# Kernel tuning notes

Hardware: AMD Instinct MI355X
Metric: run time of the kernel (lower is better)

Reference implementation:

```python
import jax, jax.numpy as jnp
import numpy as np

N, T, D, C = 32, 512, 1024, 120
EPS = 1e-12
SCALE = 2.0 * (D ** 0.5)


def setup_inputs() -> dict:
    key = jax.random.key(0)
    ks = jax.random.split(key, 16)
    inp = {
        'anc_perm_input': jax.random.normal(ks[0], (N, T, D), dtype=jnp.float32),
        'pos_perm_input': jax.random.normal(ks[1], (N, T, D), dtype=jnp.float32),
        'neg_perm_input': jax.random.normal(ks[2], (N, T, D), dtype=jnp.float32),
        'anc_src_key_padding_mask': jax.random.randint(ks[3], (N, T), 0, 2) == 1,
        'pos_src_key_padding_mask': jax.random.randint(ks[4], (N, T), 0, 2) == 1,
        'neg_src_key_padding_mask': jax.random.randint(ks[5], (N, T), 0, 2) == 1,
        # learned parameters (stored as (in, out); math-equivalent to torch x @ W.T)
        'W_attn': jax.random.normal(ks[6], (D, D), dtype=jnp.float32) * 0.02,
        'b_attn': jnp.zeros((D,), dtype=jnp.float32),
        'W1': jax.random.normal(ks[7], (D, D), dtype=jnp.float32) * 0.02,
        'b1': jnp.zeros((D,), dtype=jnp.float32),
        'W2': jax.random.normal(ks[8], (D, D), dtype=jnp.float32) * 0.02,
        'b2': jnp.zeros((D,), dtype=jnp.float32),
        'ln_g': jnp.ones((D,), dtype=jnp.float32),
        'ln_b': jnp.zeros((D,), dtype=jnp.float32),
        'W_last': jax.random.normal(ks[9], (D, C), dtype=jnp.float32) * 0.02,
        'b_last': jnp.zeros((C,), dtype=jnp.float32),
    }
    return inp


def _ntd_nd(x, mask, W_attn, b_attn, W1, b1, W2, b2, ln_g, ln_b, W_last, b_last):
    # x: (N,T,D); mask: (N,T) bool, True = padding
    w = x @ W_attn + b_attn                                   # (N,T,D)
    valid = ~mask                                             # (N,T)
    scores = jnp.einsum('btd,bsd->bts', w, w)                 # (N,T,T)
    scores = jnp.where(valid[:, :, None] & valid[:, None, :], scores, 0.0)
    s = jnp.sum(scores, axis=1) / SCALE                       # (N,T)
    s = jnp.where(mask, -jnp.inf, s)
    attn = jax.nn.softmax(s, axis=1)                          # (N,T)
    # proj_head: duplicate OrderedDict key => linear1 -> relu -> linear2 (no final act)
    proj = jax.nn.relu(x @ W1 + b1) @ W2 + b2                 # (N,T,D)
    pooled = jnp.einsum('bt,btd->bd', attn, proj)             # (N,D)
    mu = jnp.mean(pooled, axis=-1, keepdims=True)
    var = jnp.var(pooled, axis=-1, keepdims=True)
    normed = (pooled - mu) / jnp.sqrt(var + EPS) * ln_g + ln_b
    return jax.nn.relu(normed) @ W_last + b_last              # (N,C)


def reference(anc_perm_input, pos_perm_input, neg_perm_input,
              anc_src_key_padding_mask, pos_src_key_padding_mask, neg_src_key_padding_mask,
              W_attn, b_attn, W1, b1, W2, b2, ln_g, ln_b, W_last, b_last):
    params = (W_attn, b_attn, W1, b1, W2, b2, ln_g, ln_b, W_last, b_last)
    anc = _ntd_nd(anc_perm_input, anc_src_key_padding_mask, *params)
    pos = _ntd_nd(pos_perm_input, pos_src_key_padding_mask, *params)
    neg = _ntd_nd(neg_perm_input, neg_src_key_padding_mask, *params)
    return (anc, pos, neg)
```

## Files before the change

### kernel.cpp

```cpp
#include <hip/hip_runtime.h>
#include <hip/hip_bf16.h>
#include <math.h>

#define N_B 32
#define T_S 512
#define D_D 1024
#define C_C 120
#define ZB 96
#define SCALE 64.0f

typedef unsigned short u16;
typedef __attribute__((ext_vector_type(8))) short short8;
typedef __attribute__((ext_vector_type(8))) unsigned short ushort8;
typedef __attribute__((ext_vector_type(4))) float floatx4;

__device__ inline u16 f2bf(float f) {
    union { __hip_bfloat16 h; u16 u; } c; c.h = __float2bfloat16(f); return c.u;
}
__device__ inline float bf2f(u16 u) {
    union { unsigned i; float f; } c; c.i = ((unsigned)u) << 16; return c.f;
}

__device__ inline void gll16(const void* g, void* l) {
    __builtin_amdgcn_global_load_lds((const __attribute__((address_space(1))) void*)g,
                                     (__attribute__((address_space(3))) void*)l,
                                     16, 0, 0);
}

__device__ inline bool mask_is_i8(const int* mk) {
    bool i8 = false;
#pragma unroll
    for (int i = 0; i < 16; i++) {
        unsigned v = ((const unsigned*)mk)[i];
        if (v > 1u) i8 = true;
    }
    return i8;
}
__device__ inline int mask_val(const int* mk, int idx, bool i8) {
    return i8 ? (int)((const signed char*)mk)[idx] : mk[idx];
}

__global__ void k_scan(const int* m0, const int* m1, const int* m2,
                       int* __restrict__ chunk_base, int* __restrict__ cnts,
                       u16* __restrict__ xp, float4* __restrict__ zreg) {
    int zb = blockIdx.x;
    int tid = threadIdx.x;
    {
        float4 zz4 = {0.f, 0.f, 0.f, 0.f};
        for (int i = zb * 256 + tid; i < (2 * 1024 * 1024 / 16); i += ZB * 256)
            zreg[i] = zz4;
    }
    int z = zb >> 5, b = zb & 31;
    const int* mk = z == 0 ? m0 : (z == 1 ? m1 : m2);
    bool i8 = mask_is_i8(mk);
    __shared__ int wcnt[8];
    bool v0 = (mask_val(mk, b * T_S + tid, i8) == 0);
    bool v1 = (mask_val(mk, b * T_S + 256 + tid, i8) == 0);
    unsigned long long b0 = __ballot(v0);
    unsigned long long b1 = __ballot(v1);
    int wave = tid >> 6;
    if ((tid & 63) == 0) {
        wcnt[wave] = (int)__popcll(b0);
        wcnt[wave + 4] = (int)__popcll(b1);
    }
    __syncthreads();
    __shared__ int s_cnt;
    if (tid == 0) {
        int run = 0;
#pragma unroll
        for (int c = 0; c < 8; c++) {
            chunk_base[zb * 8 + c] = run;
            run += wcnt[c];
        }
        cnts[zb] = run;
        s_cnt = run;
    }
    __syncthreads();
    int cnt = s_cnt;
    int cend = (cnt + 255) & ~255;
    if (cend > T_S) cend = T_S;
    u16* base = xp + ((size_t)zb * T_S + cnt) * D_D;
    int n8 = (cend - cnt) * (D_D / 8);
    ushort8 zz = {0,0,0,0,0,0,0,0};
    for (int i = tid; i < n8; i += 256)
        *(ushort8*)(base + (size_t)i * 8) = zz;
}

__global__ void k_prep(const float* __restrict__ W_attn, const float* __restrict__ W1,
                       const float* x0, const float* x1, const float* x2,
                       const int* m0, const int* m1, const int* m2,
                       const int* __restrict__ chunk_base,
                       float* __restrict__ WT, u16* __restrict__ W1T,
                       float* __restrict__ xsum, u16* __restrict__ xp) {
    int bx = blockIdx.x;
    int tid = threadIdx.x;
    if (bx < 1024) {
        int tbx = bx & 31, tby = bx >> 5;
        __shared__ float tile[32][33];
        int tx = tid & 31, ty = tid >> 5;
#pragma unroll
        for (int j = 0; j < 32; j += 8)
            tile[ty + j][tx] = W_attn[(size_t)(tby*32 + ty + j)*D_D + tbx*32 + tx];
        __syncthreads();
#pragma unroll
        for (int j = 0; j < 32; j += 8)
            WT[(size_t)(tbx*32 + ty + j)*D_D + tby*32 + tx] = tile[tx][ty + j];
        __syncthreads();
#pragma unroll
        for (int j = 0; j < 32; j += 8)
            tile[ty + j][tx] = W1[(size_t)(tby*32 + ty + j)*D_D + tbx*32 + tx];
        __syncthreads();
#pragma unroll
        for (int j = 0; j < 32; j += 8)
            W1T[(size_t)(tbx*32 + ty + j)*D_D + tby*32 + tx] = f2bf(tile[tx][ty + j]);
        return;
    }
    int idx = bx - 1024;
    int chunk = idx & 7, zb = idx >> 3;
    int z = zb >> 5, b = zb & 31;
    const float* x = z == 0 ? x0 : (z == 1 ? x1 : x2);
    const int* mk = z == 0 ? m0 : (z == 1 ? m1 : m2);
    bool i8 = mask_is_i8(mk);
    int t0 = chunk * 64;
    __shared__ unsigned char s_list[64];
    __shared__ int s_cc;
    if (tid < 64) {
        bool v = (mask_val(mk, b * T_S + t0 + tid, i8) == 0);
        unsigned long long bal = __ballot(v);
        int pos = (int)__popcll(bal & ((1ull << tid) - 1ull));
        if (v) s_list[pos] = (unsigned char)tid;
        if (tid == 0) s_cc = (int)__popcll(bal);
    }
    __syncthreads();
    int cc = s_cc;
    int slot0 = chunk_base[zb * 8 + chunk];
    const float4* xr = (const float4*)(x + (size_t)(b * T_S) * D_D);
    u16* pack = xp + (size_t)zb * T_S * D_D;
    float4 acc = {0.f, 0.f, 0.f, 0.f};
#pragma unroll 2
    for (int j = 0; j < cc; j++) {
        int t = t0 + (int)s_list[j];
        float4 v = xr[(size_t)t * 256 + tid];
        union { __hip_bfloat162 h; ushort2 u; } c0, c1;
        c0.h = __float22bfloat162_rn({v.x, v.y});
        c1.h = __float22bfloat162_rn({v.z, v.w});
        ushort4 uu = {c0.u.x, c0.u.y, c1.u.x, c1.u.y};
        *(ushort4*)(pack + (size_t)(slot0 + j) * D_D + tid * 4) = uu;
        acc.x += v.x; acc.y += v.y; acc.z += v.z; acc.w += v.w;
    }
    float* xs = xsum + (size_t)zb * D_D + tid * 4;
    atomicAdd(xs + 0, acc.x); atomicAdd(xs + 1, acc.y);
    atomicAdd(xs + 2, acc.z); atomicAdd(xs + 3, acc.w);
}

__global__ void k_matvec(const float* __restrict__ W, const float* __restrict__ vin,
                         const float* __restrict__ bias, const int* __restrict__ bmul,
                         float scale, float* __restrict__ vout) {
    int z = blockIdx.z, bg = blockIdx.y;
    int och = blockIdx.x >> 3, kc = blockIdx.x & 7;
    int o = och * 256 + threadIdx.x;
    int brow = z * N_B + bg * 4;
    float acc[4] = {0.f, 0.f, 0.f, 0.f};
    if (kc == 0 && bias) {
        float bv = bias[o];
#pragma unroll
        for (int bb = 0; bb < 4; bb++)
            acc[bb] = bmul ? bv * (float)bmul[brow + bb] : bv;
    }
    const float* vi = vin + (size_t)brow * D_D + kc * 128;
    const float* Wp = W + (size_t)(kc * 128) * D_D + o;
#pragma unroll 4
    for (int i = 0; i < 128; i++) {
        float wv = Wp[(size_t)i * D_D];
#pragma unroll
        for (int bb = 0; bb < 4; bb++)
            acc[bb] += vi[(size_t)bb * D_D + i] * wv;
    }
#pragma unroll
    for (int bb = 0; bb < 4; bb++)
        atomicAdd(&vout[(size_t)(brow + bb) * D_D + o], acc[bb] * scale);
}

__global__ void k_dots(const u16* __restrict__ xp, const float* __restrict__ vs,
                       const int* __restrict__ cnts, float* __restrict__ sdot) {
    int zb = blockIdx.y;
    int t0 = blockIdx.x * 4;
    if (t0 >= cnts[zb]) return;
    int t = t0 + (threadIdx.x >> 6);
    int lane = threadIdx.x & 63;
    const u16* xr = xp + ((size_t)zb * T_S + t) * D_D;
    const float* vr = vs + (size_t)zb * D_D;
    float acc = 0.f;
#pragma unroll
    for (int i = 0; i < 2; i++) {
        short8 v = *(const short8*)(xr + i * 512 + lane * 8);
        const float* vp = vr + i * 512 + lane * 8;
        float4 a0 = *(const float4*)(vp);
        float4 a1 = *(const float4*)(vp + 4);
        acc += bf2f((u16)v[0]) * a0.x + bf2f((u16)v[1]) * a0.y
             + bf2f((u16)v[2]) * a0.z + bf2f((u16)v[3]) * a0.w
             + bf2f((u16)v[4]) * a1.x + bf2f((u16)v[5]) * a1.y
             + bf2f((u16)v[6]) * a1.z + bf2f((u16)v[7]) * a1.w;
    }
#pragma unroll
    for (int off = 32; off; off >>= 1) acc += __shfl_xor(acc, off, 64);
    if (lane == 0) sdot[(size_t)zb * T_S + t] = acc;
}

#define STAGE_TILE(buf, k0)                                                   \
    {                                                                         \
        _Pragma("unroll")                                                     \
        for (int i_ = 0; i_ < 4; i_++) {                                      \
            int r0_ = i_ * 64 + wave * 8;                                     \
            int rr_ = r0_ + srow;                                             \
            int gc_ = cp ^ srow;            \
            gll16(abase + (size_t)rr_ * D_D + (k0) + gc_ * 8,                 \
                  &As[buf][r0_ * 64]);                                        \
            gll16(bbase + (size_t)rr_ * D_D + (k0) + gc_ * 8,                 \
                  &Bs[buf][r0_ * 64]);                                        \
        }                                                                     \
    }

__global__ __launch_bounds__(512, 2)
void k_gemm_bf16(const u16* __restrict__ xp, const u16* __restrict__ W1T,
                 const float* __restrict__ b1, const float* __restrict__ sdot,
                 const int* __restrict__ cnts, float* __restrict__ r) {
    int flat = blockIdx.x;
    int sub = flat & 7, zb = flat >> 3;
    int Mt = sub >> 2, Nt = sub & 3;
    int row0 = Mt * 256, N0 = Nt * 256;
    int cnt = cnts[zb];
    if (row0 >= cnt) return;

    __shared__ __align__(16) u16 As[2][256 * 64];
    __shared__ __align__(16) u16 Bs[2][256 * 64];
    __shared__ float sAttn[256];
    __shared__ float redm[8], reds[8];
    int tid = threadIdx.x;
    int wave = tid >> 6, lane = tid & 63;

    {
        int base = zb * T_S;
        float v = (tid < cnt) ? sdot[base + tid] : -INFINITY;
        float mx = v;
#pragma unroll
        for (int off = 32; off; off >>= 1) mx = fmaxf(mx, __shfl_xor(mx, off, 64));
        if (lane == 0) redm[wave] = mx;
        __syncthreads();
        mx = redm[0];
#pragma unroll
        for (int k = 1; k < 8; k++) mx = fmaxf(mx, redm[k]);
        float e = __expf(v - mx);
#pragma unroll
        for (int off = 32; off; off >>= 1) e += __shfl_xor(e, off, 64);
        if (lane == 0) reds[wave] = e;
        __syncthreads();
        float tot = 0.f;
#pragma unroll
        for (int k = 0; k < 8; k++) tot += reds[k];
        if (tid < 256) {
            int t = row0 + tid;
            float av = 0.f;
            if (t < cnt) av = __expf(sdot[base + t] - mx) / tot;
            sAttn[tid] = av;
        }
    }

    int wy = wave >> 2, wx = wave & 3;
    int q = lane >> 4, cidx = lane & 15;
    int srow = lane >> 3;
    int cp = lane & 7;

    floatx4 acc[8][4];
#pragma unroll
    for (int mi = 0; mi < 8; mi++)
#pragma unroll
        for (int ni = 0; ni < 4; ni++)
            acc[mi][ni] = (floatx4){0.f, 0.f, 0.f, 0.f};

    const u16* abase = xp + ((size_t)zb * T_S + row0) * D_D;
    const u16* bbase = W1T + (size_t)N0 * D_D;

    STAGE_TILE(0, 0)
    __syncthreads();
    int cur = 0;
#pragma unroll 2
    for (int kt = 0; kt < 16; kt++) {
        if (kt < 15) { STAGE_TILE(cur ^ 1, (kt + 1) << 6) }
        __builtin_amdgcn_sched_barrier(0);
#pragma unroll
        for (int ks = 0; ks < 2; ks++) {
            short8 a[8], bfr[4];
#pragma unroll
            for (int mi = 0; mi < 8; mi++) {
                int m = wy * 128 + mi * 16 + cidx;
                a[mi] = *(const short8*)&As[cur][m * 64 + ((((ks << 2) | q) ^ (m & 7)) << 3)];
            }
#pragma unroll
            for (int ni = 0; ni < 4; ni++) {
                int n = wx * 64 + ni * 16 + cidx;
                bfr[ni] = *(const short8*)&Bs[cur][n * 64 + ((((ks << 2) | q) ^ (n & 7)) << 3)];
            }
#pragma unroll
            for (int mi = 0; mi < 8; mi++)
#pragma unroll
                for (int ni = 0; ni < 4; ni++)
                    acc[mi][ni] = __builtin_amdgcn_mfma_f32_16x16x32_bf16(
                        a[mi], bfr[ni], acc[mi][ni], 0, 0, 0);
        }
        __syncthreads();
        cur ^= 1;
    }

    float* rrow = r + (size_t)zb * D_D;
#pragma unroll
    for (int ni = 0; ni < 4; ni++) {
        int ng = N0 + wx * 64 + ni * 16 + cidx;
        float b1v = b1[ng];
        float sum = 0.f;
#pragma unroll
        for (int mi = 0; mi < 8; mi++) {
#pragma unroll
            for (int rg = 0; rg < 4; rg++) {
                int ml = wy * 128 + mi * 16 + q * 4 + rg;
                float hv = acc[mi][ni][rg] + b1v;
                hv = fmaxf(hv, 0.f);
                sum += hv * sAttn[ml];
            }
        }
        sum += __shfl_xor(sum, 16, 64);
        sum += __shfl_xor(sum, 32, 64);
        if (lane < 16) atomicAdd(&rrow[ng], sum);
    }
}

__global__ void k_pool(const float* __restrict__ rbuf, const float* __restrict__ W2,
                       const float* __restrict__ b2, float* __restrict__ pooled) {
    int zb = blockIdx.y;
    int och = blockIdx.x >> 3, kc = blockIdx.x & 7;
    int o = och * 256 + threadIdx.x;
    float acc = (kc == 0) ? b2[o] : 0.f;
    const float* rp = rbuf + (size_t)zb * D_D + kc * 128;
    const float* Wp = W2 + (size_t)(kc * 128) * D_D + o;
#pragma unroll 4
    for (int i = 0; i < 128; i++)
        acc += rp[i] * Wp[(size_t)i * D_D];
    atomicAdd(&pooled[(size_t)zb * D_D + o], acc);
}

__global__ void k_fin(const float* __restrict__ pooled, const float* __restrict__ ln_g,
                      const float* __restrict__ ln_b, const float* __restrict__ Wl,
                      const float* __restrict__ bl, float* __restrict__ out) {
    int zb = blockIdx.x;
    int tid = threadIdx.x;
    __shared__ float nr[D_D];
    __shared__ float redA[8], redB[8];
    __shared__ float ps[4][C_C];
    const float* p = pooled + (size_t)zb * D_D;
    int o0 = tid, o1 = tid + 512;
    float a0 = p[o0], a1 = p[o1];
    float s1 = a0 + a1, s2 = a0 * a0 + a1 * a1;
#pragma unroll
    for (int off = 32; off; off >>= 1) {
        s1 += __shfl_xor(s1, off, 64);
        s2 += __shfl_xor(s2, off, 64);
    }
    int w = tid >> 6;
    if ((tid & 63) == 0) { redA[w] = s1; redB[w] = s2; }
    __syncthreads();
    float t1 = 0.f, t2 = 0.f;
#pragma unroll
    for (int k = 0; k < 8; k++) { t1 += redA[k]; t2 += redB[k]; }
    float mu = t1 * (1.0f / D_D);
    float var = t2 * (1.0f / D_D) - mu * mu;
    float rstd = 1.0f / sqrtf(var + 1e-12f);
    nr[o0] = fmaxf((a0 - mu) * rstd * ln_g[o0] + ln_b[o0], 0.f);
    nr[o1] = fmaxf((a1 - mu) * rstd * ln_g[o1] + ln_b[o1], 0.f);
    __syncthreads();
    if (tid < 4 * C_C) {
        int seg = tid / C_C, c = tid - seg * C_C;
        const float* wp = Wl + (size_t)(seg * 256) * C_C + c;
        const float* np = nr + seg * 256;
        float acc = 0.f;
#pragma unroll 8
        for (int d = 0; d < 256; d++)
            acc += np[d] * wp[(size_t)d * C_C];
        ps[seg][c] = acc;
    }
    __syncthreads();
    if (tid < C_C)
        out[(size_t)zb * C_C + tid] =
            bl[tid] + ps[0][tid] + ps[1][tid] + ps[2][tid] + ps[3][tid];
}

extern "C" void kernel_launch(void* const* d_in, const int* in_sizes, int n_in,
                              void* d_out, int out_size, void* d_ws, size_t ws_size,
                              hipStream_t stream) {
    const float* x0 = (const float*)d_in[0];
    const float* x1 = (const float*)d_in[1];
    const float* x2 = (const float*)d_in[2];
    const int* m0 = (const int*)d_in[3];
    const int* m1 = (const int*)d_in[4];
    const int* m2 = (const int*)d_in[5];
    const float* W_attn = (const float*)d_in[6];
    const float* b_attn = (const float*)d_in[7];
    const float* W1 = (const float*)d_in[8];
    const float* b1 = (const float*)d_in[9];
    const float* W2 = (const float*)d_in[10];
    const float* b2 = (const float*)d_in[11];
    const float* ln_g = (const float*)d_in[12];
    const float* ln_b = (const float*)d_in[13];
    const float* W_last = (const float*)d_in[14];
    const float* b_last = (const float*)d_in[15];
    float* out = (float*)d_out;

    char* wsb = (char*)d_ws;
    const size_t MB = 1 << 20;
    float* WT     = (float*)(wsb);
    u16*   W1T    = (u16*)  (wsb + 4 * MB);
    float* xsum   = (float*)(wsb + 6 * MB);
    float* rbuf   = (float*)(wsb + 6 * MB + 393216);
    float* wsum   = (float*)(wsb + 6 * MB + 786432);
    float* vs     = (float*)(wsb + 6 * MB + 1179648);
    float* pooled = (float*)(wsb + 6 * MB + 1572864);
    float* sdot   = (float*)(wsb + 8 * MB);
    int*   cbase  = (int*)  (wsb + 8 * MB + 196608);
    int*   cnts   = (int*)  (wsb + 8 * MB + 199680);
    u16*   xp     = (u16*)  (wsb + 9 * MB);

    k_scan  <<<ZB, 256, 0, stream>>>(m0, m1, m2, cbase, cnts, xp,
                                     (float4*)(wsb + 6 * MB));
    k_prep  <<<1792, 256, 0, stream>>>(W_attn, W1, x0, x1, x2, m0, m1, m2,
                                       cbase, WT, W1T, xsum, xp);
    k_matvec<<<dim3(32, 8, 3), 256, 0, stream>>>(W_attn, xsum, b_attn, cnts, 1.0f, wsum);
    k_matvec<<<dim3(32, 8, 3), 256, 0, stream>>>(WT, wsum, nullptr, nullptr, 1.0f / SCALE, vs);
    k_dots  <<<dim3(128, ZB), 256, 0, stream>>>(xp, vs, cnts, sdot);
    k_gemm_bf16<<<768, 512, 0, stream>>>(xp, W1T, b1, sdot, cnts, rbuf);
    k_pool  <<<dim3(32, ZB), 256, 0, stream>>>(rbuf, W2, b2, pooled);
    k_fin   <<<ZB, 512, 0, stream>>>(pooled, ln_g, ln_b, W_last, b_last, out);
}
```

Measured before the change: 401.3 us.

## Use 128-row tiles with triple-buffered LDS pipeline in bf16 GEMM

The GEMM tile shrinks from 256x256 to 128x256, so padding work is trimmed at a finer row granularity and the grid doubles. The double-buffered loop becomes a 3-stage LDS ring with explicit vmcnt waits and barriers. MFMA sections are raised with setprio, and block indices are remapped so blocks sharing a W1 column tile are adjacent. Occupancy drops to one block per CU because of the larger LDS footprint. The explicit wait counts must match the number of loads issued per stage.

```diff
diff --git a/kernel.cpp b/kernel.cpp
--- a/kernel.cpp
+++ b/kernel.cpp
@@ -26,6 +26,9 @@
                                      (__attribute__((address_space(3))) void*)l,
                                      16, 0, 0);
 }
+
+#define VMW(n) asm volatile("s_waitcnt vmcnt(" #n ")" ::: "memory")
+#define LGW()  asm volatile("s_waitcnt lgkmcnt(0)" ::: "memory")
 
 __device__ inline bool mask_is_i8(const int* mk) {
     bool i8 = false;
@@ -77,7 +80,7 @@
     }
     __syncthreads();
     int cnt = s_cnt;
-    int cend = (cnt + 255) & ~255;
+    int cend = (cnt + 127) & ~127;
     if (cend > T_S) cend = T_S;
     u16* base = xp + ((size_t)zb * T_S + cnt) * D_D;
     int n8 = (cend - cnt) * (D_D / 8);
@@ -207,34 +210,39 @@
     if (lane == 0) sdot[(size_t)zb * T_S + t] = acc;
 }
 
-#define STAGE_TILE(buf, k0)                                                   \
+
+#define STAGE3(s, kt)                                                         \
     {                                                                         \
+        int k0_ = (kt) << 6;                                                  \
         _Pragma("unroll")                                                     \
-        for (int i_ = 0; i_ < 4; i_++) {                                      \
-            int r0_ = i_ * 64 + wave * 8;                                     \
-            int rr_ = r0_ + srow;                                             \
-            int gc_ = cp ^ srow;            \
-            gll16(abase + (size_t)rr_ * D_D + (k0) + gc_ * 8,                 \
-                  &As[buf][r0_ * 64]);                                        \
-            gll16(bbase + (size_t)rr_ * D_D + (k0) + gc_ * 8,                 \
-                  &Bs[buf][r0_ * 64]);                                        \
+        for (int j_ = 0; j_ < 2; j_++) {                                      \
+            int rr_ = wave * 16 + j_ * 8 + srow;                              \
+            gll16(abase + (size_t)rr_ * D_D + k0_ + (cp ^ srow) * 8,          \
+                  &As[s][(wave * 16 + j_ * 8) * 64]);                         \
         }                                                                     \
-    }
-
-__global__ __launch_bounds__(512, 2)
+        _Pragma("unroll")                                                     \
+        for (int j_ = 0; j_ < 4; j_++) {                                      \
+            int nn_ = wave * 32 + j_ * 8 + srow;                              \
+            gll16(bbase + (size_t)nn_ * D_D + k0_ + (cp ^ srow) * 8,          \
+                  &Bs[s][(wave * 32 + j_ * 8) * 64]);                         \
+        }                                                                     \
+    }
+
+__global__ __launch_bounds__(512, 1)
 void k_gemm_bf16(const u16* __restrict__ xp, const u16* __restrict__ W1T,
                  const float* __restrict__ b1, const float* __restrict__ sdot,
                  const int* __restrict__ cnts, float* __restrict__ r) {
-    int flat = blockIdx.x;
-    int sub = flat & 7, zb = flat >> 3;
-    int Mt = sub >> 2, Nt = sub & 3;
-    int row0 = Mt * 256, N0 = Nt * 256;
+    int idx = blockIdx.x;
+    int nt = (idx >> 3) & 3;
+    int rest = (idx & 7) | ((idx >> 5) << 3);
+    int zb = rest >> 2, mt = rest & 3;
+    int row0 = mt * 128, N0 = nt * 256;
     int cnt = cnts[zb];
     if (row0 >= cnt) return;
 
-    __shared__ __align__(16) u16 As[2][256 * 64];
-    __shared__ __align__(16) u16 Bs[2][256 * 64];
-    __shared__ float sAttn[256];
+    __shared__ __align__(16) u16 As[3][128 * 64];
+    __shared__ __align__(16) u16 Bs[3][256 * 64];
+    __shared__ float sAttn[128];
     __shared__ float redm[8], reds[8];
     int tid = threadIdx.x;
     int wave = tid >> 6, lane = tid & 63;
@@ -258,12 +266,13 @@
         float tot = 0.f;
 #pragma unroll
         for (int k = 0; k < 8; k++) tot += reds[k];
-        if (tid < 256) {
+        if (tid < 128) {
             int t = row0 + tid;
             float av = 0.f;
             if (t < cnt) av = __expf(sdot[base + t] - mx) / tot;
             sAttn[tid] = av;
         }
+        __syncthreads();
     }
 
     int wy = wave >> 2, wx = wave & 3;
@@ -271,9 +280,9 @@
     int srow = lane >> 3;
     int cp = lane & 7;
 
-    floatx4 acc[8][4];
-#pragma unroll
-    for (int mi = 0; mi < 8; mi++)
+    floatx4 acc[4][4];
+#pragma unroll
+    for (int mi = 0; mi < 4; mi++)
 #pragma unroll
         for (int ni = 0; ni < 4; ni++)
             acc[mi][ni] = (floatx4){0.f, 0.f, 0.f, 0.f};
@@ -281,35 +290,47 @@
     const u16* abase = xp + ((size_t)zb * T_S + row0) * D_D;
     const u16* bbase = W1T + (size_t)N0 * D_D;
 
-    STAGE_TILE(0, 0)
-    __syncthreads();
-    int cur = 0;
-#pragma unroll 2
-    for (int kt = 0; kt < 16; kt++) {
-        if (kt < 15) { STAGE_TILE(cur ^ 1, (kt + 1) << 6) }
-        __builtin_amdgcn_sched_barrier(0);
-#pragma unroll
-        for (int ks = 0; ks < 2; ks++) {
-            short8 a[8], bfr[4];
-#pragma unroll
-            for (int mi = 0; mi < 8; mi++) {
-                int m = wy * 128 + mi * 16 + cidx;
-                a[mi] = *(const short8*)&As[cur][m * 64 + ((((ks << 2) | q) ^ (m & 7)) << 3)];
-            }
-#pragma unroll
-            for (int ni = 0; ni < 4; ni++) {
-                int n = wx * 64 + ni * 16 + cidx;
-                bfr[ni] = *(const short8*)&Bs[cur][n * 64 + ((((ks << 2) | q) ^ (n & 7)) << 3)];
-            }
-#pragma unroll
-            for (int mi = 0; mi < 8; mi++)
-#pragma unroll
-                for (int ni = 0; ni < 4; ni++)
+    STAGE3(0, 0)
+    STAGE3(1, 1)
+    STAGE3(2, 2)
+    VMW(12);
+    __builtin_amdgcn_s_barrier();
+
+#pragma unroll
+    for (int t = 0; t < 16; t++) {
+        int sl = t % 3;
+        short8 a[4][2], b[4][2];
+#pragma unroll
+        for (int mi = 0; mi < 4; mi++) {
+            int m = wy * 64 + mi * 16 + cidx;
+#pragma unroll
+            for (int ks = 0; ks < 2; ks++)
+                a[mi][ks] = *(const short8*)&As[sl][m * 64 + ((((ks << 2) | q) ^ (m & 7)) << 3)];
+        }
+#pragma unroll
+        for (int ni = 0; ni < 4; ni++) {
+            int n = wx * 64 + ni * 16 + cidx;
+#pragma unroll
+            for (int ks = 0; ks < 2; ks++)
+                b[ni][ks] = *(const short8*)&Bs[sl][n * 64 + ((((ks << 2) | q) ^ (n & 7)) << 3)];
+        }
+        LGW();
+        __builtin_amdgcn_s_barrier();
+        if (t < 13) { STAGE3(sl, t + 3) }
+        if (t < 13)      { VMW(12); }
+        else if (t == 13){ VMW(6);  }
+        else if (t == 14){ VMW(0);  }
+        __builtin_amdgcn_s_barrier();
+        __builtin_amdgcn_s_setprio(1);
+#pragma unroll
+        for (int mi = 0; mi < 4; mi++)
+#pragma unroll
+            for (int ni = 0; ni < 4; ni++)
+#pragma unroll
+                for (int ks = 0; ks < 2; ks++)
                     acc[mi][ni] = __builtin_amdgcn_mfma_f32_16x16x32_bf16(
-                        a[mi], bfr[ni], acc[mi][ni], 0, 0, 0);
-        }
-        __syncthreads();
-        cur ^= 1;
+                        a[mi][ks], b[ni][ks], acc[mi][ni], 0, 0, 0);
+        __builtin_amdgcn_s_setprio(0);
     }
 
     float* rrow = r + (size_t)zb * D_D;
@@ -319,10 +340,10 @@
         float b1v = b1[ng];
         float sum = 0.f;
 #pragma unroll
-        for (int mi = 0; mi < 8; mi++) {
+        for (int mi = 0; mi < 4; mi++) {
 #pragma unroll
             for (int rg = 0; rg < 4; rg++) {
-                int ml = wy * 128 + mi * 16 + q * 4 + rg;
+                int ml = wy * 64 + mi * 16 + q * 4 + rg;
                 float hv = acc[mi][ni][rg] + b1v;
                 hv = fmaxf(hv, 0.f);
                 sum += hv * sAttn[ml];
@@ -435,7 +456,7 @@
     k_matvec<<<dim3(32, 8, 3), 256, 0, stream>>>(W_attn, xsum, b_attn, cnts, 1.0f, wsum);
     k_matvec<<<dim3(32, 8, 3), 256, 0, stream>>>(WT, wsum, nullptr, nullptr, 1.0f / SCALE, vs);
     k_dots  <<<dim3(128, ZB), 256, 0, stream>>>(xp, vs, cnts, sdot);
-    k_gemm_bf16<<<768, 512, 0, stream>>>(xp, W1T, b1, sdot, cnts, rbuf);
+    k_gemm_bf16<<<1536, 512, 0, stream>>>(xp, W1T, b1, sdot, cnts, rbuf);
     k_pool  <<<dim3(32, ZB), 256, 0, stream>>>(rbuf, W2, b2, pooled);
     k_fin   <<<ZB, 512, 0, stream>>>(pooled, ln_g, ln_b, W_last, b_last, out);
 }
```

After: 411.9 us. 2.6% more time.

## Pack valid tokens globally across batches to cut padded GEMM work

Applied to the files above, without the earlier changes.

Valid rows of all 96 sequences are now packed contiguously, each padded only to a multiple of 64 instead of 256 per sequence. A block-to-sequence map lets the GEMM tiles span several sequences. Softmax is moved out of the GEMM into its own kernel, so the redundant per-tile recomputation goes away. k_pool is replaced by the batched matvec. This reduces the wasted MFMA work on padded rows at 256-row granularity, at the cost of a serial prefix scan in every k_scan block, an extra launch, and launch bounds lowered from 2 blocks per CU to 1.

```diff
diff --git a/kernel.cpp b/kernel.cpp
--- a/kernel.cpp
+++ b/kernel.cpp
@@ -41,8 +41,10 @@
 }
 
 __global__ void k_scan(const int* m0, const int* m1, const int* m2,
-                       int* __restrict__ chunk_base, int* __restrict__ cnts,
-                       u16* __restrict__ xp, float4* __restrict__ zreg) {
+                       int* __restrict__ slotbase, int* __restrict__ cnts,
+                       int* __restrict__ gb, int* __restrict__ zblk,
+                       int* __restrict__ mtot, u16* __restrict__ xp,
+                       float* __restrict__ attnw, float4* __restrict__ zreg) {
     int zb = blockIdx.x;
     int tid = threadIdx.x;
     {
@@ -50,46 +52,72 @@
         for (int i = zb * 256 + tid; i < (2 * 1024 * 1024 / 16); i += ZB * 256)
             zreg[i] = zz4;
     }
-    int z = zb >> 5, b = zb & 31;
-    const int* mk = z == 0 ? m0 : (z == 1 ? m1 : m2);
-    bool i8 = mask_is_i8(mk);
-    __shared__ int wcnt[8];
-    bool v0 = (mask_val(mk, b * T_S + tid, i8) == 0);
-    bool v1 = (mask_val(mk, b * T_S + 256 + tid, i8) == 0);
-    unsigned long long b0 = __ballot(v0);
-    unsigned long long b1 = __ballot(v1);
+    bool i8_0 = mask_is_i8(m0), i8_1 = mask_is_i8(m1), i8_2 = mask_is_i8(m2);
+    __shared__ unsigned short wc[ZB][8];
+    __shared__ int scnt[ZB], sgb[ZB], stot;
     int wave = tid >> 6;
-    if ((tid & 63) == 0) {
-        wcnt[wave] = (int)__popcll(b0);
-        wcnt[wave + 4] = (int)__popcll(b1);
-    }
-    __syncthreads();
-    __shared__ int s_cnt;
+#pragma unroll 4
+    for (int zb2 = 0; zb2 < ZB; zb2++) {
+        int z2 = zb2 >> 5, b2 = zb2 & 31;
+        const int* mk = z2 == 0 ? m0 : (z2 == 1 ? m1 : m2);
+        bool i8 = z2 == 0 ? i8_0 : (z2 == 1 ? i8_1 : i8_2);
+        bool v0 = (mask_val(mk, b2 * T_S + tid, i8) == 0);
+        bool v1 = (mask_val(mk, b2 * T_S + 256 + tid, i8) == 0);
+        unsigned long long bl0 = __ballot(v0);
+        unsigned long long bl1 = __ballot(v1);
+        if ((tid & 63) == 0) {
+            wc[zb2][wave] = (unsigned short)__popcll(bl0);
+            wc[zb2][wave + 4] = (unsigned short)__popcll(bl1);
+        }
+    }
+    __syncthreads();
+    if (tid < ZB) {
+        int s = 0;
+#pragma unroll
+        for (int c = 0; c < 8; c++) s += wc[tid][c];
+        scnt[tid] = s;
+    }
+    __syncthreads();
     if (tid == 0) {
         int run = 0;
-#pragma unroll
-        for (int c = 0; c < 8; c++) {
-            chunk_base[zb * 8 + c] = run;
-            run += wcnt[c];
-        }
-        cnts[zb] = run;
-        s_cnt = run;
-    }
-    __syncthreads();
-    int cnt = s_cnt;
-    int cend = (cnt + 255) & ~255;
-    if (cend > T_S) cend = T_S;
-    u16* base = xp + ((size_t)zb * T_S + cnt) * D_D;
-    int n8 = (cend - cnt) * (D_D / 8);
-    ushort8 zz = {0,0,0,0,0,0,0,0};
-    for (int i = tid; i < n8; i += 256)
-        *(ushort8*)(base + (size_t)i * 8) = zz;
+        for (int i = 0; i < ZB; i++) { sgb[i] = run; run += (scnt[i] + 63) & ~63; }
+        stot = run;
+    }
+    __syncthreads();
+    int cnt = scnt[zb], base = sgb[zb];
+    if (tid == 0) {
+        cnts[zb] = cnt; gb[zb] = base;
+        int run = base;
+#pragma unroll
+        for (int c = 0; c < 8; c++) { slotbase[zb * 8 + c] = run; run += wc[zb][c]; }
+        if (zb == ZB - 1) mtot[0] = stot;
+    }
+    int nb = (cnt + 63) >> 6;
+    if (tid < nb) zblk[(base >> 6) + tid] = zb;
+    int cend = (cnt + 63) & ~63;
+    {
+        u16* bp = xp + (size_t)(base + cnt) * D_D;
+        int n8 = (cend - cnt) * (D_D / 8);
+        ushort8 zz = {0,0,0,0,0,0,0,0};
+        for (int i = tid; i < n8; i += 256)
+            *(ushort8*)(bp + (size_t)i * 8) = zz;
+    }
+    if (zb == ZB - 1) {
+        int tot = stot, tend = (tot + 255) & ~255;
+        u16* bp = xp + (size_t)tot * D_D;
+        int n8 = (tend - tot) * (D_D / 8);
+        ushort8 zz = {0,0,0,0,0,0,0,0};
+        for (int i = tid; i < n8; i += 256)
+            *(ushort8*)(bp + (size_t)i * 8) = zz;
+        for (int i = tid; i < tend - tot; i += 256) attnw[tot + i] = 0.f;
+        if (tid < ((tend - tot) >> 6)) zblk[(tot >> 6) + tid] = 0;
+    }
 }
 
 __global__ void k_prep(const float* __restrict__ W_attn, const float* __restrict__ W1,
                        const float* x0, const float* x1, const float* x2,
                        const int* m0, const int* m1, const int* m2,
-                       const int* __restrict__ chunk_base,
+                       const int* __restrict__ slotbase,
                        float* __restrict__ WT, u16* __restrict__ W1T,
                        float* __restrict__ xsum, u16* __restrict__ xp) {
     int bx = blockIdx.x;
@@ -133,9 +161,8 @@
     }
     __syncthreads();
     int cc = s_cc;
-    int slot0 = chunk_base[zb * 8 + chunk];
+    int slot0 = slotbase[zb * 8 + chunk];
     const float4* xr = (const float4*)(x + (size_t)(b * T_S) * D_D);
-    u16* pack = xp + (size_t)zb * T_S * D_D;
     float4 acc = {0.f, 0.f, 0.f, 0.f};
 #pragma unroll 2
     for (int j = 0; j < cc; j++) {
@@ -145,7 +172,7 @@
         c0.h = __float22bfloat162_rn({v.x, v.y});
         c1.h = __float22bfloat162_rn({v.z, v.w});
         ushort4 uu = {c0.u.x, c0.u.y, c1.u.x, c1.u.y};
-        *(ushort4*)(pack + (size_t)(slot0 + j) * D_D + tid * 4) = uu;
+        *(ushort4*)(xp + (size_t)(slot0 + j) * D_D + tid * 4) = uu;
         acc.x += v.x; acc.y += v.y; acc.z += v.z; acc.w += v.w;
     }
     float* xs = xsum + (size_t)zb * D_D + tid * 4;
@@ -182,13 +209,14 @@
 }
 
 __global__ void k_dots(const u16* __restrict__ xp, const float* __restrict__ vs,
-                       const int* __restrict__ cnts, float* __restrict__ sdot) {
-    int zb = blockIdx.y;
+                       const int* __restrict__ zblk, const int* __restrict__ mtot,
+                       float* __restrict__ sdot) {
     int t0 = blockIdx.x * 4;
-    if (t0 >= cnts[zb]) return;
+    if (t0 >= mtot[0]) return;
     int t = t0 + (threadIdx.x >> 6);
     int lane = threadIdx.x & 63;
-    const u16* xr = xp + ((size_t)zb * T_S + t) * D_D;
+    int zb = zblk[t0 >> 6];
+    const u16* xr = xp + (size_t)t * D_D;
     const float* vr = vs + (size_t)zb * D_D;
     float acc = 0.f;
 #pragma unroll
@@ -204,7 +232,35 @@
     }
 #pragma unroll
     for (int off = 32; off; off >>= 1) acc += __shfl_xor(acc, off, 64);
-    if (lane == 0) sdot[(size_t)zb * T_S + t] = acc;
+    if (lane == 0) sdot[t] = acc;
+}
+
+__global__ void k_smax(const float* __restrict__ sdot, const int* __restrict__ cnts,
+                       const int* __restrict__ gb, float* __restrict__ attnw) {
+    int zb = blockIdx.x, tid = threadIdx.x;
+    __shared__ float redm[8], reds[8];
+    int cnt = cnts[zb], base = gb[zb];
+    int wave = tid >> 6, lane = tid & 63;
+    float v = (tid < cnt) ? sdot[base + tid] : -INFINITY;
+    float mx = v;
+#pragma unroll
+    for (int off = 32; off; off >>= 1) mx = fmaxf(mx, __shfl_xor(mx, off, 64));
+    if (lane == 0) redm[wave] = mx;
+    __syncthreads();
+    mx = redm[0];
+#pragma unroll
+    for (int k = 1; k < 8; k++) mx = fmaxf(mx, redm[k]);
+    float e = __expf(v - mx);
+    float es = e;
+#pragma unroll
+    for (int off = 32; off; off >>= 1) es += __shfl_xor(es, off, 64);
+    if (lane == 0) reds[wave] = es;
+    __syncthreads();
+    float tot = 0.f;
+#pragma unroll
+    for (int k = 0; k < 8; k++) tot += reds[k];
+    int cend = (cnt + 63) & ~63;
+    if (tid < cend) attnw[base + tid] = (tid < cnt) ? (e / tot) : 0.f;
 }
 
 #define STAGE_TILE(buf, k0)                                                   \
@@ -221,50 +277,24 @@
         }                                                                     \
     }
 
-__global__ __launch_bounds__(512, 2)
+__global__ __launch_bounds__(512, 1)
 void k_gemm_bf16(const u16* __restrict__ xp, const u16* __restrict__ W1T,
-                 const float* __restrict__ b1, const float* __restrict__ sdot,
-                 const int* __restrict__ cnts, float* __restrict__ r) {
-    int flat = blockIdx.x;
-    int sub = flat & 7, zb = flat >> 3;
-    int Mt = sub >> 2, Nt = sub & 3;
+                 const float* __restrict__ b1, const float* __restrict__ attnw,
+                 const int* __restrict__ zblk, const int* __restrict__ mtot,
+                 float* __restrict__ rbuf) {
+    int bid = blockIdx.x;
+    int sub = bid & 31;
+    int Mt = (bid >> 5) * 8 + (sub & 7);
+    int Nt = sub >> 3;
     int row0 = Mt * 256, N0 = Nt * 256;
-    int cnt = cnts[zb];
-    if (row0 >= cnt) return;
+    if (row0 >= mtot[0]) return;
 
     __shared__ __align__(16) u16 As[2][256 * 64];
     __shared__ __align__(16) u16 Bs[2][256 * 64];
     __shared__ float sAttn[256];
-    __shared__ float redm[8], reds[8];
     int tid = threadIdx.x;
     int wave = tid >> 6, lane = tid & 63;
-
-    {
-        int base = zb * T_S;
-        float v = (tid < cnt) ? sdot[base + tid] : -INFINITY;
-        float mx = v;
-#pragma unroll
-        for (int off = 32; off; off >>= 1) mx = fmaxf(mx, __shfl_xor(mx, off, 64));
-        if (lane == 0) redm[wave] = mx;
-        __syncthreads();
-        mx = redm[0];
-#pragma unroll
-        for (int k = 1; k < 8; k++) mx = fmaxf(mx, redm[k]);
-        float e = __expf(v - mx);
-#pragma unroll
-        for (int off = 32; off; off >>= 1) e += __shfl_xor(e, off, 64);
-        if (lane == 0) reds[wave] = e;
-        __syncthreads();
-        float tot = 0.f;
-#pragma unroll
-        for (int k = 0; k < 8; k++) tot += reds[k];
-        if (tid < 256) {
-            int t = row0 + tid;
-            float av = 0.f;
-            if (t < cnt) av = __expf(sdot[base + t] - mx) / tot;
-            sAttn[tid] = av;
-        }
-    }
+    if (tid < 256) sAttn[tid] = attnw[row0 + tid];
 
     int wy = wave >> 2, wx = wave & 3;
     int q = lane >> 4, cidx = lane & 15;
@@ -278,7 +308,7 @@
         for (int ni = 0; ni < 4; ni++)
             acc[mi][ni] = (floatx4){0.f, 0.f, 0.f, 0.f};
 
-    const u16* abase = xp + ((size_t)zb * T_S + row0) * D_D;
+    const u16* abase = xp + (size_t)row0 * D_D;
     const u16* bbase = W1T + (size_t)N0 * D_D;
 
     STAGE_TILE(0, 0)
@@ -312,40 +342,31 @@
         cur ^= 1;
     }
 
-    float* rrow = r + (size_t)zb * D_D;
+    int zb0 = zblk[(row0 >> 6) + wy * 2];
+    int zb1 = zblk[(row0 >> 6) + wy * 2 + 1];
 #pragma unroll
     for (int ni = 0; ni < 4; ni++) {
         int ng = N0 + wx * 64 + ni * 16 + cidx;
         float b1v = b1[ng];
-        float sum = 0.f;
+        float s0 = 0.f, s1 = 0.f;
 #pragma unroll
         for (int mi = 0; mi < 8; mi++) {
+            float part = 0.f;
 #pragma unroll
             for (int rg = 0; rg < 4; rg++) {
                 int ml = wy * 128 + mi * 16 + q * 4 + rg;
-                float hv = acc[mi][ni][rg] + b1v;
-                hv = fmaxf(hv, 0.f);
-                sum += hv * sAttn[ml];
+                float hv = fmaxf(acc[mi][ni][rg] + b1v, 0.f);
+                part += hv * sAttn[ml];
             }
+            if (mi < 4) s0 += part; else s1 += part;
         }
-        sum += __shfl_xor(sum, 16, 64);
-        sum += __shfl_xor(sum, 32, 64);
-        if (lane < 16) atomicAdd(&rrow[ng], sum);
-    }
-}
-
-__global__ void k_pool(const float* __restrict__ rbuf, const float* __restrict__ W2,
-                       const float* __restrict__ b2, float* __restrict__ pooled) {
-    int zb = blockIdx.y;
-    int och = blockIdx.x >> 3, kc = blockIdx.x & 7;
-    int o = och * 256 + threadIdx.x;
-    float acc = (kc == 0) ? b2[o] : 0.f;
-    const float* rp = rbuf + (size_t)zb * D_D + kc * 128;
-    const float* Wp = W2 + (size_t)(kc * 128) * D_D + o;
-#pragma unroll 4
-    for (int i = 0; i < 128; i++)
-        acc += rp[i] * Wp[(size_t)i * D_D];
-    atomicAdd(&pooled[(size_t)zb * D_D + o], acc);
+        s0 += __shfl_xor(s0, 16, 64); s0 += __shfl_xor(s0, 32, 64);
+        s1 += __shfl_xor(s1, 16, 64); s1 += __shfl_xor(s1, 32, 64);
+        if (lane < 16) {
+            atomicAdd(&rbuf[(size_t)zb0 * D_D + ng], s0);
+            atomicAdd(&rbuf[(size_t)zb1 * D_D + ng], s1);
+        }
+    }
 }
 
 __global__ void k_fin(const float* __restrict__ pooled, const float* __restrict__ ln_g,
@@ -424,18 +445,23 @@
     float* vs     = (float*)(wsb + 6 * MB + 1179648);
     float* pooled = (float*)(wsb + 6 * MB + 1572864);
     float* sdot   = (float*)(wsb + 8 * MB);
-    int*   cbase  = (int*)  (wsb + 8 * MB + 196608);
-    int*   cnts   = (int*)  (wsb + 8 * MB + 199680);
+    float* attnw  = (float*)(wsb + 8 * MB + 196608);
+    int*   slotb  = (int*)  (wsb + 8 * MB + 393216);
+    int*   cnts   = (int*)  (wsb + 8 * MB + 397312);
+    int*   gb     = (int*)  (wsb + 8 * MB + 401408);
+    int*   mtot   = (int*)  (wsb + 8 * MB + 405504);
+    int*   zblk   = (int*)  (wsb + 8 * MB + 409600);
     u16*   xp     = (u16*)  (wsb + 9 * MB);
 
-    k_scan  <<<ZB, 256, 0, stream>>>(m0, m1, m2, cbase, cnts, xp,
-                                     (float4*)(wsb + 6 * MB));
+    k_scan  <<<ZB, 256, 0, stream>>>(m0, m1, m2, slotb, cnts, gb, zblk, mtot,
+                                     xp, attnw, (float4*)(wsb + 6 * MB));
     k_prep  <<<1792, 256, 0, stream>>>(W_attn, W1, x0, x1, x2, m0, m1, m2,
-                                       cbase, WT, W1T, xsum, xp);
+                                       slotb, WT, W1T, xsum, xp);
     k_matvec<<<dim3(32, 8, 3), 256, 0, stream>>>(W_attn, xsum, b_attn, cnts, 1.0f, wsum);
     k_matvec<<<dim3(32, 8, 3), 256, 0, stream>>>(WT, wsum, nullptr, nullptr, 1.0f / SCALE, vs);
-    k_dots  <<<dim3(128, ZB), 256, 0, stream>>>(xp, vs, cnts, sdot);
-    k_gemm_bf16<<<768, 512, 0, stream>>>(xp, W1T, b1, sdot, cnts, rbuf);
-    k_pool  <<<dim3(32, ZB), 256, 0, stream>>>(rbuf, W2, b2, pooled);
+    k_dots  <<<12288, 256, 0, stream>>>(xp, vs, zblk, mtot, sdot);
+    k_smax  <<<ZB, 512, 0, stream>>>(sdot, cnts, gb, attnw);
+    k_gemm_bf16<<<768, 512, 0, stream>>>(xp, W1T, b1, attnw, zblk, mtot, rbuf);
+    k_matvec<<<dim3(32, 8, 3), 256, 0, stream>>>(W2, rbuf, b2, nullptr, 1.0f, pooled);
     k_fin   <<<ZB, 512, 0, stream>>>(pooled, ln_g, ln_b, W_last, b_last, out);
 }
```

Measured after the change: 406.0 us. About the same (+1.2%).
